# Kernel tuning notes

Measured on AMD Instinct MI355X. Metric: run time of the kernel, lower is better.

## Reference

```python
import jax, jax.numpy as jnp
import numpy as np
import math

DIM = 256
LEVELS = [8, 8, 8, 8]
CODEBOOK_SIZE = int(math.prod(LEVELS))  # 4096
COMMIT_W = 0.25
B, N = 8, 2048


def setup_inputs() -> dict:
    key = jax.random.key(0)
    kx, kc = jax.random.split(key)
    x = jax.random.normal(kx, (B, DIM, N), dtype=jnp.float32)
    # nn.init.normal_(std=1/sqrt(dim))
    codebook = jax.random.normal(kc, (CODEBOOK_SIZE, DIM), dtype=jnp.float32) / math.sqrt(DIM)
    return {"x": x, "codebook": codebook}


def reference(x, codebook):
    # x: [B, dim, N] -> x_bnd: [B, N, dim]
    x_bnd = jnp.transpose(x, (0, 2, 1))
    flat_x = x_bnd.reshape(-1, DIM)  # [B*N, dim]
    distances = (
        jnp.sum(flat_x * flat_x, axis=-1, keepdims=True)
        - 2.0 * flat_x @ codebook.T
        + jnp.sum(codebook * codebook, axis=-1)[None, :]
    )  # [B*N, K]
    indices = jnp.argmin(distances, axis=-1).reshape(B, N)  # int
    quantized_bnd = codebook[indices]  # [B, N, dim] gather
    # commitment loss (quantized detached)
    commit_loss = jnp.mean((jax.lax.stop_gradient(quantized_bnd) - x_bnd) ** 2) * COMMIT_W
    # straight-through estimator
    st = x_bnd + jax.lax.stop_gradient(quantized_bnd - x_bnd)
    quantized = jnp.transpose(st, (0, 2, 1))  # back to [B, dim, N]
    return quantized, indices, commit_loss
```

## Files before the change

kernel.cpp:

```cpp
#include <hip/hip_runtime.h>
#include <float.h>

#define DIM      256
#define KCODES   4096
#define NSEQ     2048
#define IDXOFF   4194304
#define LOSS_OFF 4210688
#define NTILE    64
#define THRESH   1.0e-3f
#define RCAP     1024

typedef __attribute__((ext_vector_type(8))) short short8;
typedef __attribute__((ext_vector_type(4))) float f32x4;

__device__ __forceinline__ void bsplit(float x, unsigned short& hi, unsigned short& lo) {
  union { float f; unsigned u; } a; a.f = x;
  unsigned r = a.u + 0x7FFFu + ((a.u >> 16) & 1u);
  hi = (unsigned short)(r >> 16);
  union { unsigned u; float f; } h; h.u = ((unsigned)hi) << 16;
  float res = x - h.f;
  union { float f; unsigned u; } b2; b2.f = res;
  unsigned r2 = b2.u + 0x7FFFu + ((b2.u >> 16) & 1u);
  lo = (unsigned short)(r2 >> 16);
}

__device__ __forceinline__ void gload_lds16(const void* g, void* l) {
  __builtin_amdgcn_global_load_lds(
      (const __attribute__((address_space(1))) unsigned*)g,
      (__attribute__((address_space(3))) unsigned*)l, 16, 0, 0);
}

__global__ __launch_bounds__(256) void fsq_prep(const float* __restrict__ cb,
                                                float* __restrict__ cn32,
                                                double* __restrict__ cn64,
                                                double* __restrict__ wsloss,
                                                int* __restrict__ rcount) {
  int code = blockIdx.x * 256 + threadIdx.x;
  const float4* c4 = reinterpret_cast<const float4*>(cb + (size_t)code * DIM);
  double s = 0.0;
#pragma unroll 8
  for (int i = 0; i < DIM / 4; ++i) {
    float4 v = c4[i];
    s += (double)v.x * v.x + (double)v.y * v.y + (double)v.z * v.z + (double)v.w * v.w;
  }
  cn32[code] = (float)s;
  cn64[code] = s;
  if (code == 0) { *wsloss = 0.0; *rcount = 0; }
}

__global__ __launch_bounds__(256) void fsq_perm(const float* __restrict__ cb,
                                                char* __restrict__ cbsplit) {
  int tid = blockIdx.x * 256 + threadIdx.x;
  int ti  = tid >> 11;
  int c   = tid & 2047;
  int frag = c >> 6, ll = c & 63;
  int chh = frag >> 4, stt = (frag >> 1) & 7, cgg = frag & 1;
  int kgg = ll >> 4,  coll = ll & 15;
  int code  = ti * 64 + chh * 32 + cgg * 16 + coll;
  int dbase = stt * 32 + kgg * 8;
  const float4* p = (const float4*)(cb + (size_t)code * DIM + dbase);
  float4 aa = p[0], bb = p[1];
  float vv[8] = {aa.x, aa.y, aa.z, aa.w, bb.x, bb.y, bb.z, bb.w};
  short8 h8, l8;
#pragma unroll
  for (int j = 0; j < 8; ++j) {
    unsigned short hh, lo2;
    bsplit(vv[j], hh, lo2);
    h8[j] = (short)hh; l8[j] = (short)lo2;
  }
  *(short8*)(cbsplit + (size_t)ti * 65536 + c * 16) = h8;
  *(short8*)(cbsplit + (size_t)ti * 65536 + 32768 + c * 16) = l8;
}

__global__ __launch_bounds__(512, 2) void fsq_score(
    const float* __restrict__ x, const float* __restrict__ cb,
    const char* __restrict__ cbsplit, const float* __restrict__ cn32,
    int* __restrict__ idxws, int* __restrict__ rcount, int* __restrict__ rlist,
    float* __restrict__ out, double* __restrict__ wsloss) {
  __shared__ __align__(16) short tiles[2][32768];
  __shared__ float m1[8][16], m2[8][16];
  __shared__ int   mi[8][16];
  __shared__ int   sIdx[64];
  __shared__ double wl[8];

  const int t   = threadIdx.x;
  const int wid = t >> 6;
  const int l   = t & 63;
  const int col = l & 15;
  const int kg  = l >> 4;
  const int rg  = wid & 3;
  const int ch  = wid >> 2;
  const int g0  = blockIdx.x * 64;
  const int b   = g0 >> 11;
  const int n0  = g0 & (NSEQ - 1);

  short8 ahi[8], alo[8];
  {
    const float* xb = x + (size_t)(b << 8) * NSEQ + (n0 + rg * 16 + col);
#pragma unroll
    for (int st = 0; st < 8; ++st) {
      short8 h8, l8;
#pragma unroll
      for (int j = 0; j < 8; ++j) {
        float v = xb[(size_t)(st * 32 + kg * 8 + j) * NSEQ];
        unsigned short hh, ll2;
        bsplit(v, hh, ll2);
        h8[j] = (short)hh; l8[j] = (short)ll2;
      }
      ahi[st] = h8; alo[st] = l8;
    }
  }

#pragma unroll
  for (int s = 0; s < 8; ++s)
    gload_lds16(cbsplit + s * 8192 + wid * 1024 + (l << 4),
                (char*)&tiles[0][0] + s * 8192 + wid * 1024);
  __syncthreads();

  float v1[4], v2[4]; int i1[4];
#pragma unroll
  for (int r = 0; r < 4; ++r) { v1[r] = FLT_MAX; v2[r] = FLT_MAX; i1[r] = 0; }

  int cur = 0;
  for (int ti = 0; ti < NTILE; ++ti) {
    if (ti + 1 < NTILE) {
      const char* src = cbsplit + (size_t)(ti + 1) * 65536;
#pragma unroll
      for (int s = 0; s < 8; ++s)
        gload_lds16(src + s * 8192 + wid * 1024 + (l << 4),
                    (char*)&tiles[cur ^ 1][0] + s * 8192 + wid * 1024);
    }

    f32x4 acc[2] = {{0, 0, 0, 0}, {0, 0, 0, 0}};
    const char* base = (const char*)&tiles[cur][0] + ch * 16384 + (l << 4);
#pragma unroll
    for (int st = 0; st < 8; ++st) {
#pragma unroll
      for (int cg = 0; cg < 2; ++cg) {
        const char* p = base + st * 2048 + cg * 1024;
        short8 bh = *(const short8*)p;
        short8 bl = *(const short8*)(p + 32768);
        acc[cg] = __builtin_amdgcn_mfma_f32_16x16x32_bf16(ahi[st], bh, acc[cg], 0, 0, 0);
        acc[cg] = __builtin_amdgcn_mfma_f32_16x16x32_bf16(alo[st], bh, acc[cg], 0, 0, 0);
        acc[cg] = __builtin_amdgcn_mfma_f32_16x16x32_bf16(ahi[st], bl, acc[cg], 0, 0, 0);
      }
    }

#pragma unroll
    for (int cg = 0; cg < 2; ++cg) {
      int k = ti * 64 + ch * 32 + cg * 16 + col;
      float cn = cn32[k];
#pragma unroll
      for (int r = 0; r < 4; ++r) {
        float dist = fmaf(-2.f, acc[cg][r], cn);
        if (dist < v1[r]) { v2[r] = v1[r]; v1[r] = dist; i1[r] = k; }
        else              { v2[r] = fminf(v2[r], dist); }
      }
    }
    __syncthreads();
    cur ^= 1;
  }

#pragma unroll
  for (int r = 0; r < 4; ++r) {
    float a1 = v1[r], a2 = v2[r]; int ai = i1[r];
#pragma unroll
    for (int off = 1; off < 16; off <<= 1) {
      float o1 = __shfl_xor(a1, off, 64);
      float o2 = __shfl_xor(a2, off, 64);
      int   oi = __shfl_xor(ai, off, 64);
      if (o1 < a1 || (o1 == a1 && oi < ai)) { a2 = fminf(a1, o2); a1 = o1; ai = oi; }
      else                                  { a2 = fminf(a2, o1); }
    }
    v1[r] = a1; v2[r] = a2; i1[r] = ai;
  }
  if (col == 0) {
#pragma unroll
    for (int r = 0; r < 4; ++r) {
      m1[wid][kg * 4 + r] = v1[r];
      m2[wid][kg * 4 + r] = v2[r];
      mi[wid][kg * 4 + r] = i1[r];
    }
  }
  __syncthreads();

  if (t < 64) {
    int rgg = t >> 4, li = t & 15;
    float a1 = m1[rgg][li], a2 = m2[rgg][li]; int ai = mi[rgg][li];
    float o1 = m1[rgg + 4][li], o2 = m2[rgg + 4][li]; int oi = mi[rgg + 4][li];
    if (o1 < a1 || (o1 == a1 && oi < ai)) { a2 = fminf(a1, o2); a1 = o1; ai = oi; }
    else                                  { a2 = fminf(a2, o1); }
    bool flag = (a2 - a1) < THRESH;
    sIdx[t] = ai;
    idxws[g0 + t] = flag ? -(ai + 1) : ai;
    out[IDXOFF + g0 + t] = (float)ai;
    if (flag) { int p = atomicAdd(rcount, 1); if (p < RCAP) rlist[p] = g0 + t; }
  }
  __syncthreads();

  float* qt = (float*)&tiles[0][0];
  {
    int r = t >> 3, seg = t & 7;
    const float4* cp = (const float4*)(cb + (size_t)sIdx[r] * DIM + seg * 32);
#pragma unroll
    for (int i = 0; i < 8; ++i) {
      float4 v = cp[i];
      int d = seg * 32 + i * 4;
      qt[r * 257 + d]     = v.x;
      qt[r * 257 + d + 1] = v.y;
      qt[r * 257 + d + 2] = v.z;
      qt[r * 257 + d + 3] = v.w;
    }
  }
  __syncthreads();

  float lsum = 0.f;
  {
    int r = t & 63, part = t >> 6;
    const float* xp = x   + (size_t)((b << 8) + part * 32) * NSEQ + n0 + r;
    float*       op = out + (size_t)((b << 8) + part * 32) * NSEQ + n0 + r;
#pragma unroll
    for (int i = 0; i < 32; ++i) {
      float qv = qt[r * 257 + part * 32 + i];
      float xv = xp[(size_t)i * NSEQ];
      op[(size_t)i * NSEQ] = qv;
      float dx = qv - xv;
      lsum = fmaf(dx, dx, lsum);
    }
  }
#pragma unroll
  for (int off = 32; off > 0; off >>= 1) lsum += __shfl_xor(lsum, off, 64);
  if (l == 0) wl[wid] = (double)lsum;
  __syncthreads();
  if (t == 0) {
    double s = 0.0;
#pragma unroll
    for (int w = 0; w < 8; ++w) s += wl[w];
    atomicAdd(wsloss, s);
  }
}

__global__ __launch_bounds__(256) void fsq_rescreen(
    const float* __restrict__ x, const float* __restrict__ cb,
    const double* __restrict__ cn64, const int* __restrict__ rcount,
    const int* __restrict__ rlist, const int* __restrict__ idxws,
    float* __restrict__ out, double* __restrict__ wsloss) {
  __shared__ float  xrow[DIM];
  __shared__ double rv[4];
  __shared__ int    ri[4];
  __shared__ int    sBi;
  __shared__ double dl[4];

  const int t    = threadIdx.x;
  const int lane = t & 63;
  const int wv   = t >> 6;
  int cnt = *rcount;
  if (cnt > RCAP) cnt = RCAP;
  if (cnt < 0) cnt = 0;

  for (int i = blockIdx.x; i < cnt; i += gridDim.x) {
    const int row = rlist[i] & 16383;
    const int b   = row >> 11;
    const int n   = row & (NSEQ - 1);
    xrow[t] = x[((size_t)(b << 8) + t) * NSEQ + n];
    __syncthreads();

    double best = DBL_MAX;
    int    bi   = 0;
    const float4* xr = reinterpret_cast<const float4*>(&xrow[0]);
#pragma unroll 1
    for (int c = 0; c < 16; ++c) {
      int k = t + (c << 8);
      const float4* cp = reinterpret_cast<const float4*>(cb + (size_t)k * DIM);
      double dot = 0.0;
#pragma unroll 4
      for (int d4 = 0; d4 < DIM / 4; ++d4) {
        float4 cv = cp[d4];
        float4 xv = xr[d4];
        dot += (double)xv.x * cv.x + (double)xv.y * cv.y +
               (double)xv.z * cv.z + (double)xv.w * cv.w;
      }
      double dist = cn64[k] - 2.0 * dot;
      if (dist < best || (dist == best && k < bi)) { best = dist; bi = k; }
    }
#pragma unroll
    for (int off = 1; off < 64; off <<= 1) {
      double ob = __shfl_xor(best, off, 64);
      int    oi = __shfl_xor(bi, off, 64);
      if (ob < best || (ob == best && oi < bi)) { best = ob; bi = oi; }
    }
    if (lane == 0) { rv[wv] = best; ri[wv] = bi; }
    __syncthreads();
    if (t == 0) {
      double bb = rv[0]; int ii = ri[0];
#pragma unroll
      for (int w = 1; w < 4; ++w)
        if (rv[w] < bb || (rv[w] == bb && ri[w] < ii)) { bb = rv[w]; ii = ri[w]; }
      sBi = ii;
    }
    __syncthreads();

    int enc = idxws[row];
    int old = (enc < 0) ? -(enc + 1) : enc;
    int nw  = sBi;
    if (nw != old) {
      if (t == 0) out[IDXOFF + row] = (float)nw;
      float qn = cb[(size_t)nw  * DIM + t];
      float qo = cb[(size_t)old * DIM + t];
      float xv = xrow[t];
      out[((size_t)(b << 8) + t) * NSEQ + n] = qn;
      float d1 = qn - xv, d0 = qo - xv;
      float delta = d1 * d1 - d0 * d0;
#pragma unroll
      for (int off = 32; off > 0; off >>= 1) delta += __shfl_xor(delta, off, 64);
      if (lane == 0) dl[wv] = (double)delta;
      __syncthreads();
      if (t == 0) atomicAdd(wsloss, dl[0] + dl[1] + dl[2] + dl[3]);
    }
    __syncthreads();
  }
}

__global__ void fsq_finish(const double* __restrict__ wsloss, float* __restrict__ out) {
  if (threadIdx.x == 0)
    out[LOSS_OFF] = (float)(*wsloss * (0.25 / 4194304.0));
}

extern "C" void kernel_launch(void* const* d_in, const int* in_sizes, int n_in,
                              void* d_out, int out_size, void* d_ws, size_t ws_size,
                              hipStream_t stream) {
  const float* x  = (const float*)d_in[0];
  const float* cb = (const float*)d_in[1];
  float* out = (float*)d_out;

  char* wsb = (char*)d_ws;
  double* wsloss = (double*)wsb;
  int*    rcount = (int*)(wsb + 8);
  float*  cn32   = (float*)(wsb + 4096);
  double* cn64   = (double*)(wsb + 4096 + 16384);
  int*    idxws  = (int*)(wsb + 4096 + 16384 + 32768);
  int*    rlist  = (int*)(wsb + 4096 + 16384 + 32768 + 65536);
  char*   cbsplit = wsb + 131072;

  fsq_prep<<<KCODES / 256, 256, 0, stream>>>(cb, cn32, cn64, wsloss, rcount);
  fsq_perm<<<512, 256, 0, stream>>>(cb, cbsplit);
  fsq_score<<<256, 512, 0, stream>>>(x, cb, cbsplit, cn32, idxws, rcount, rlist, out, wsloss);
  fsq_rescreen<<<256, 256, 0, stream>>>(x, cb, cn64, rcount, rlist, idxws, out, wsloss);
  fsq_finish<<<1, 64, 0, stream>>>(wsloss, out);
}
```

Baseline: 335.2 us.

## Retile score kernel so each wave reuses B fragments across two row groups

The score kernel's wave layout changes from 4 row groups × 2 code halves to 2 row groups × 4 code quarters. Each wave now holds A fragments for 32 rows and reuses each loaded codebook fragment across two accumulators, which halves the LDS reads per MFMA, and the codebook split layout is permuted to match. The prep and perm kernels are merged into one launch. The double-precision loss workspace and finish kernel are dropped in favour of float atomics scaled directly into the output. This adds register pressure from the doubled A fragments and makes the loss accumulation order-dependent in float.

Result: no change. 336.2 us (+0.3%).

```diff
diff --git a/kernel.cpp b/kernel.cpp
--- a/kernel.cpp
+++ b/kernel.cpp
@@ -9,9 +9,11 @@
 #define NTILE    64
 #define THRESH   1.0e-3f
 #define RCAP     1024
+#define LOSS_SCALE (0.25f / 4194304.0f)
 
 typedef __attribute__((ext_vector_type(8))) short short8;
 typedef __attribute__((ext_vector_type(4))) float f32x4;
+typedef __attribute__((ext_vector_type(4))) unsigned short us4;
 
 __device__ __forceinline__ void bsplit(float x, unsigned short& hi, unsigned short& lo) {
   union { float f; unsigned u; } a; a.f = x;
@@ -31,72 +33,77 @@
 }
 
 __global__ __launch_bounds__(256) void fsq_prep(const float* __restrict__ cb,
+                                                char* __restrict__ cbsplit,
                                                 float* __restrict__ cn32,
                                                 double* __restrict__ cn64,
-                                                double* __restrict__ wsloss,
-                                                int* __restrict__ rcount) {
-  int code = blockIdx.x * 256 + threadIdx.x;
-  const float4* c4 = reinterpret_cast<const float4*>(cb + (size_t)code * DIM);
-  double s = 0.0;
+                                                int* __restrict__ rcount,
+                                                float* __restrict__ out) {
+  const int bid = blockIdx.x;
+  const int t   = threadIdx.x;
+  if (bid < 512) {
+    int tid = bid * 256 + t;
+    int ti  = tid >> 11;
+    int c   = tid & 2047;
+    int st  = c >> 8;
+    int ch  = (c >> 6) & 3;
+    int l   = c & 63;
+    int kg  = l >> 4, col = l & 15;
+    int code  = ti * 64 + ch * 16 + col;
+    int dbase = st * 32 + kg * 8;
+    const float4* p = (const float4*)(cb + (size_t)code * DIM + dbase);
+    float4 aa = p[0], bb = p[1];
+    float vv[8] = {aa.x, aa.y, aa.z, aa.w, bb.x, bb.y, bb.z, bb.w};
+    short8 h8, l8;
+#pragma unroll
+    for (int j = 0; j < 8; ++j) {
+      unsigned short hh, lo2;
+      bsplit(vv[j], hh, lo2);
+      h8[j] = (short)hh; l8[j] = (short)lo2;
+    }
+    char* tb = cbsplit + (size_t)ti * 65536 + (c >> 6) * 2048 + l * 16;
+    *(short8*)tb = h8;
+    *(short8*)(tb + 1024) = l8;
+  } else {
+    int code = (bid - 512) * 256 + t;
+    const float4* c4 = reinterpret_cast<const float4*>(cb + (size_t)code * DIM);
+    double s = 0.0;
 #pragma unroll 8
-  for (int i = 0; i < DIM / 4; ++i) {
-    float4 v = c4[i];
-    s += (double)v.x * v.x + (double)v.y * v.y + (double)v.z * v.z + (double)v.w * v.w;
-  }
-  cn32[code] = (float)s;
-  cn64[code] = s;
-  if (code == 0) { *wsloss = 0.0; *rcount = 0; }
-}
-
-__global__ __launch_bounds__(256) void fsq_perm(const float* __restrict__ cb,
-                                                char* __restrict__ cbsplit) {
-  int tid = blockIdx.x * 256 + threadIdx.x;
-  int ti  = tid >> 11;
-  int c   = tid & 2047;
-  int frag = c >> 6, ll = c & 63;
-  int chh = frag >> 4, stt = (frag >> 1) & 7, cgg = frag & 1;
-  int kgg = ll >> 4,  coll = ll & 15;
-  int code  = ti * 64 + chh * 32 + cgg * 16 + coll;
-  int dbase = stt * 32 + kgg * 8;
-  const float4* p = (const float4*)(cb + (size_t)code * DIM + dbase);
-  float4 aa = p[0], bb = p[1];
-  float vv[8] = {aa.x, aa.y, aa.z, aa.w, bb.x, bb.y, bb.z, bb.w};
-  short8 h8, l8;
-#pragma unroll
-  for (int j = 0; j < 8; ++j) {
-    unsigned short hh, lo2;
-    bsplit(vv[j], hh, lo2);
-    h8[j] = (short)hh; l8[j] = (short)lo2;
-  }
-  *(short8*)(cbsplit + (size_t)ti * 65536 + c * 16) = h8;
-  *(short8*)(cbsplit + (size_t)ti * 65536 + 32768 + c * 16) = l8;
+    for (int i = 0; i < DIM / 4; ++i) {
+      float4 v = c4[i];
+      s += (double)v.x * v.x + (double)v.y * v.y + (double)v.z * v.z + (double)v.w * v.w;
+    }
+    cn32[code] = (float)s;
+    cn64[code] = s;
+    if (code == 0) { *rcount = 0; out[LOSS_OFF] = 0.0f; }
+  }
 }
 
 __global__ __launch_bounds__(512, 2) void fsq_score(
     const float* __restrict__ x, const float* __restrict__ cb,
     const char* __restrict__ cbsplit, const float* __restrict__ cn32,
     int* __restrict__ idxws, int* __restrict__ rcount, int* __restrict__ rlist,
-    float* __restrict__ out, double* __restrict__ wsloss) {
+    float* __restrict__ out) {
   __shared__ __align__(16) short tiles[2][32768];
-  __shared__ float m1[8][16], m2[8][16];
-  __shared__ int   mi[8][16];
+  __shared__ float m1[8][32], m2[8][32];
+  __shared__ int   mi[8][32];
   __shared__ int   sIdx[64];
-  __shared__ double wl[8];
+  __shared__ float wl[8];
 
   const int t   = threadIdx.x;
   const int wid = t >> 6;
   const int l   = t & 63;
   const int col = l & 15;
   const int kg  = l >> 4;
-  const int rg  = wid & 3;
-  const int ch  = wid >> 2;
+  const int rg  = wid >> 2;
+  const int ch  = wid & 3;
   const int g0  = blockIdx.x * 64;
   const int b   = g0 >> 11;
   const int n0  = g0 & (NSEQ - 1);
 
-  short8 ahi[8], alo[8];
-  {
-    const float* xb = x + (size_t)(b << 8) * NSEQ + (n0 + rg * 16 + col);
+  short8 ahi[2][8], alo[2][8];
+#pragma unroll
+  for (int rs = 0; rs < 2; ++rs) {
+    const float* xb = x + (size_t)(b << 8) * NSEQ + (n0 + rg * 32 + rs * 16 + col);
 #pragma unroll
     for (int st = 0; st < 8; ++st) {
       short8 h8, l8;
@@ -107,7 +114,7 @@
         bsplit(v, hh, ll2);
         h8[j] = (short)hh; l8[j] = (short)ll2;
       }
-      ahi[st] = h8; alo[st] = l8;
+      ahi[rs][st] = h8; alo[rs][st] = l8;
     }
   }
 
@@ -117,9 +124,11 @@
                 (char*)&tiles[0][0] + s * 8192 + wid * 1024);
   __syncthreads();
 
-  float v1[4], v2[4]; int i1[4];
-#pragma unroll
-  for (int r = 0; r < 4; ++r) { v1[r] = FLT_MAX; v2[r] = FLT_MAX; i1[r] = 0; }
+  float v1[2][4], v2[2][4]; int i1[2][4];
+#pragma unroll
+  for (int rs = 0; rs < 2; ++rs)
+#pragma unroll
+    for (int r = 0; r < 4; ++r) { v1[rs][r] = FLT_MAX; v2[rs][r] = FLT_MAX; i1[rs][r] = 0; }
 
   int cur = 0;
   for (int ti = 0; ti < NTILE; ++ti) {
@@ -132,64 +141,69 @@
     }
 
     f32x4 acc[2] = {{0, 0, 0, 0}, {0, 0, 0, 0}};
-    const char* base = (const char*)&tiles[cur][0] + ch * 16384 + (l << 4);
+    const char* base = (const char*)&tiles[cur][0] + (ch << 11) + (l << 4);
+    __builtin_amdgcn_s_setprio(1);
 #pragma unroll
     for (int st = 0; st < 8; ++st) {
-#pragma unroll
-      for (int cg = 0; cg < 2; ++cg) {
-        const char* p = base + st * 2048 + cg * 1024;
-        short8 bh = *(const short8*)p;
-        short8 bl = *(const short8*)(p + 32768);
-        acc[cg] = __builtin_amdgcn_mfma_f32_16x16x32_bf16(ahi[st], bh, acc[cg], 0, 0, 0);
-        acc[cg] = __builtin_amdgcn_mfma_f32_16x16x32_bf16(alo[st], bh, acc[cg], 0, 0, 0);
-        acc[cg] = __builtin_amdgcn_mfma_f32_16x16x32_bf16(ahi[st], bl, acc[cg], 0, 0, 0);
+      const char* p = base + (st << 13);
+      short8 bh = *(const short8*)p;
+      short8 bl = *(const short8*)(p + 1024);
+      acc[0] = __builtin_amdgcn_mfma_f32_16x16x32_bf16(ahi[0][st], bh, acc[0], 0, 0, 0);
+      acc[1] = __builtin_amdgcn_mfma_f32_16x16x32_bf16(ahi[1][st], bh, acc[1], 0, 0, 0);
+      acc[0] = __builtin_amdgcn_mfma_f32_16x16x32_bf16(alo[0][st], bh, acc[0], 0, 0, 0);
+      acc[1] = __builtin_amdgcn_mfma_f32_16x16x32_bf16(alo[1][st], bh, acc[1], 0, 0, 0);
+      acc[0] = __builtin_amdgcn_mfma_f32_16x16x32_bf16(ahi[0][st], bl, acc[0], 0, 0, 0);
+      acc[1] = __builtin_amdgcn_mfma_f32_16x16x32_bf16(ahi[1][st], bl, acc[1], 0, 0, 0);
+    }
+    __builtin_amdgcn_s_setprio(0);
+
+    {
+      int k = ti * 64 + ch * 16 + col;
+      float cn = cn32[k];
+#pragma unroll
+      for (int rs = 0; rs < 2; ++rs)
+#pragma unroll
+        for (int r = 0; r < 4; ++r) {
+          float dist = fmaf(-2.f, acc[rs][r], cn);
+          if (dist < v1[rs][r]) { v2[rs][r] = v1[rs][r]; v1[rs][r] = dist; i1[rs][r] = k; }
+          else                  { v2[rs][r] = fminf(v2[rs][r], dist); }
+        }
+    }
+    __syncthreads();
+    cur ^= 1;
+  }
+
+#pragma unroll
+  for (int rs = 0; rs < 2; ++rs)
+#pragma unroll
+    for (int r = 0; r < 4; ++r) {
+      float a1 = v1[rs][r], a2 = v2[rs][r]; int ai = i1[rs][r];
+#pragma unroll
+      for (int off = 1; off < 16; off <<= 1) {
+        float o1 = __shfl_xor(a1, off, 64);
+        float o2 = __shfl_xor(a2, off, 64);
+        int   oi = __shfl_xor(ai, off, 64);
+        if (o1 < a1 || (o1 == a1 && oi < ai)) { a2 = fminf(a1, o2); a1 = o1; ai = oi; }
+        else                                  { a2 = fminf(a2, o1); }
       }
-    }
-
-#pragma unroll
-    for (int cg = 0; cg < 2; ++cg) {
-      int k = ti * 64 + ch * 32 + cg * 16 + col;
-      float cn = cn32[k];
-#pragma unroll
-      for (int r = 0; r < 4; ++r) {
-        float dist = fmaf(-2.f, acc[cg][r], cn);
-        if (dist < v1[r]) { v2[r] = v1[r]; v1[r] = dist; i1[r] = k; }
-        else              { v2[r] = fminf(v2[r], dist); }
+      if (col == 0) {
+        m1[wid][rs * 16 + kg * 4 + r] = a1;
+        m2[wid][rs * 16 + kg * 4 + r] = a2;
+        mi[wid][rs * 16 + kg * 4 + r] = ai;
       }
     }
-    __syncthreads();
-    cur ^= 1;
-  }
-
-#pragma unroll
-  for (int r = 0; r < 4; ++r) {
-    float a1 = v1[r], a2 = v2[r]; int ai = i1[r];
-#pragma unroll
-    for (int off = 1; off < 16; off <<= 1) {
-      float o1 = __shfl_xor(a1, off, 64);
-      float o2 = __shfl_xor(a2, off, 64);
-      int   oi = __shfl_xor(ai, off, 64);
+  __syncthreads();
+
+  if (t < 64) {
+    int rgg = t >> 5, lrr = t & 31;
+    float a1 = m1[rgg * 4][lrr], a2 = m2[rgg * 4][lrr]; int ai = mi[rgg * 4][lrr];
+#pragma unroll
+    for (int c = 1; c < 4; ++c) {
+      float o1 = m1[rgg * 4 + c][lrr], o2 = m2[rgg * 4 + c][lrr];
+      int   oi = mi[rgg * 4 + c][lrr];
       if (o1 < a1 || (o1 == a1 && oi < ai)) { a2 = fminf(a1, o2); a1 = o1; ai = oi; }
       else                                  { a2 = fminf(a2, o1); }
     }
-    v1[r] = a1; v2[r] = a2; i1[r] = ai;
-  }
-  if (col == 0) {
-#pragma unroll
-    for (int r = 0; r < 4; ++r) {
-      m1[wid][kg * 4 + r] = v1[r];
-      m2[wid][kg * 4 + r] = v2[r];
-      mi[wid][kg * 4 + r] = i1[r];
-    }
-  }
-  __syncthreads();
-
-  if (t < 64) {
-    int rgg = t >> 4, li = t & 15;
-    float a1 = m1[rgg][li], a2 = m2[rgg][li]; int ai = mi[rgg][li];
-    float o1 = m1[rgg + 4][li], o2 = m2[rgg + 4][li]; int oi = mi[rgg + 4][li];
-    if (o1 < a1 || (o1 == a1 && oi < ai)) { a2 = fminf(a1, o2); a1 = o1; ai = oi; }
-    else                                  { a2 = fminf(a2, o1); }
     bool flag = (a2 - a1) < THRESH;
     sIdx[t] = ai;
     idxws[g0 + t] = flag ? -(ai + 1) : ai;
@@ -230,13 +244,13 @@
   }
 #pragma unroll
   for (int off = 32; off > 0; off >>= 1) lsum += __shfl_xor(lsum, off, 64);
-  if (l == 0) wl[wid] = (double)lsum;
+  if (l == 0) wl[wid] = lsum;
   __syncthreads();
   if (t == 0) {
-    double s = 0.0;
+    float s = 0.f;
 #pragma unroll
     for (int w = 0; w < 8; ++w) s += wl[w];
-    atomicAdd(wsloss, s);
+    atomicAdd(out + LOSS_OFF, s * LOSS_SCALE);
   }
 }
 
@@ -244,12 +258,12 @@
     const float* __restrict__ x, const float* __restrict__ cb,
     const double* __restrict__ cn64, const int* __restrict__ rcount,
     const int* __restrict__ rlist, const int* __restrict__ idxws,
-    float* __restrict__ out, double* __restrict__ wsloss) {
+    float* __restrict__ out) {
   __shared__ float  xrow[DIM];
   __shared__ double rv[4];
   __shared__ int    ri[4];
   __shared__ int    sBi;
-  __shared__ double dl[4];
+  __shared__ float  dl[4];
 
   const int t    = threadIdx.x;
   const int lane = t & 63;
@@ -313,17 +327,12 @@
       float delta = d1 * d1 - d0 * d0;
 #pragma unroll
       for (int off = 32; off > 0; off >>= 1) delta += __shfl_xor(delta, off, 64);
-      if (lane == 0) dl[wv] = (double)delta;
+      if (lane == 0) dl[wv] = delta;
       __syncthreads();
-      if (t == 0) atomicAdd(wsloss, dl[0] + dl[1] + dl[2] + dl[3]);
-    }
-    __syncthreads();
-  }
-}
-
-__global__ void fsq_finish(const double* __restrict__ wsloss, float* __restrict__ out) {
-  if (threadIdx.x == 0)
-    out[LOSS_OFF] = (float)(*wsloss * (0.25 / 4194304.0));
+      if (t == 0) atomicAdd(out + LOSS_OFF, (dl[0] + dl[1] + dl[2] + dl[3]) * LOSS_SCALE);
+    }
+    __syncthreads();
+  }
 }
 
 extern "C" void kernel_launch(void* const* d_in, const int* in_sizes, int n_in,
@@ -334,7 +343,6 @@
   float* out = (float*)d_out;
 
   char* wsb = (char*)d_ws;
-  double* wsloss = (double*)wsb;
   int*    rcount = (int*)(wsb + 8);
   float*  cn32   = (float*)(wsb + 4096);
   double* cn64   = (double*)(wsb + 4096 + 16384);
@@ -342,9 +350,7 @@
   int*    rlist  = (int*)(wsb + 4096 + 16384 + 32768 + 65536);
   char*   cbsplit = wsb + 131072;
 
-  fsq_prep<<<KCODES / 256, 256, 0, stream>>>(cb, cn32, cn64, wsloss, rcount);
-  fsq_perm<<<512, 256, 0, stream>>>(cb, cbsplit);
-  fsq_score<<<256, 512, 0, stream>>>(x, cb, cbsplit, cn32, idxws, rcount, rlist, out, wsloss);
-  fsq_rescreen<<<256, 256, 0, stream>>>(x, cb, cn64, rcount, rlist, idxws, out, wsloss);
-  fsq_finish<<<1, 64, 0, stream>>>(wsloss, out);
-}
+  fsq_prep<<<528, 256, 0, stream>>>(cb, cbsplit, cn32, cn64, rcount, out);
+  fsq_score<<<256, 512, 0, stream>>>(x, cb, cbsplit, cn32, idxws, rcount, rlist, out);
+  fsq_rescreen<<<64, 256, 0, stream>>>(x, cb, cn64, rcount, rlist, idxws, out);
+}
```
